# Kernel optimization log

Measured on AMD Instinct MI355X. Metric: run time of the kernel, lower is better.

The kernel has to match this reference:

```python
import jax, jax.numpy as jnp
import numpy as np

DIM = 1024
HEADS = 16
HEAD_DIM = DIM // HEADS
RANK = 4
AUDIO_DIM = 768


def _lora(x, A, B):
    # x: [..., in]; A: [rank, in]; B: [out, rank]
    return x + (x @ A.T @ B.T) * (1.0 / RANK)


def setup_inputs() -> dict:
    key = jax.random.key(0)
    ks = jax.random.split(key, 20)
    s = 0.02
    inp = {
        "x": jax.random.normal(ks[0], (1, 4096, DIM), jnp.float32),
        "audio_features": jax.random.normal(ks[1], (1, 1024, AUDIO_DIM), jnp.float32),
        "q_w": jax.random.normal(ks[2], (DIM, DIM), jnp.float32) * s,
        "q_b": jnp.zeros((DIM,), jnp.float32),
        "k_w": jax.random.normal(ks[3], (DIM, DIM), jnp.float32) * s,
        "k_b": jnp.zeros((DIM,), jnp.float32),
        "v_w": jax.random.normal(ks[4], (DIM, DIM), jnp.float32) * s,
        "v_b": jnp.zeros((DIM,), jnp.float32),
        "o_w": jax.random.normal(ks[5], (DIM, DIM), jnp.float32) * s,
        "o_b": jnp.zeros((DIM,), jnp.float32),
        "a_w": jax.random.normal(ks[6], (DIM, AUDIO_DIM), jnp.float32) * s,
        "a_b": jnp.zeros((DIM,), jnp.float32),
        "qA": jax.random.normal(ks[7], (RANK, DIM), jnp.float32) * 0.01,
        "qB": jax.random.normal(ks[8], (DIM, RANK), jnp.float32) * 0.01,
        "kA": jax.random.normal(ks[9], (RANK, DIM), jnp.float32) * 0.01,
        "kB": jax.random.normal(ks[10], (DIM, RANK), jnp.float32) * 0.01,
        "vA": jax.random.normal(ks[11], (RANK, DIM), jnp.float32) * 0.01,
        "vB": jax.random.normal(ks[12], (DIM, RANK), jnp.float32) * 0.01,
    }
    return inp


def reference(x, audio_features, q_w, q_b, k_w, k_b, v_w, v_b, o_w, o_b,
              a_w, a_b, qA, qB, kA, kB, vA, vB):
    B, N, C = x.shape
    # audio projection: Linear(768 -> dim), torch Linear is x @ W.T + b
    audio = audio_features @ a_w.T + a_b  # [B, M, C]
    M = audio.shape[1]

    q = _lora(x @ q_w.T + q_b, qA, qB)      # [B, N, C]
    k = _lora(audio @ k_w.T + k_b, kA, kB)  # [B, M, C]
    v = _lora(audio @ v_w.T + v_b, vA, vB)  # [B, M, C]

    q = q.reshape(B, N, HEADS, HEAD_DIM).transpose(0, 2, 1, 3)  # [B,H,N,d]
    k = k.reshape(B, M, HEADS, HEAD_DIM).transpose(0, 2, 1, 3)  # [B,H,M,d]
    v = v.reshape(B, M, HEADS, HEAD_DIM).transpose(0, 2, 1, 3)  # [B,H,M,d]

    scale = HEAD_DIM ** -0.5
    attn = jnp.einsum('bhnd,bhmd->bhnm', q, k) * scale  # [B,H,N,M]
    attn = jax.nn.softmax(attn, axis=-1)
    out = jnp.einsum('bhnm,bhmd->bhnd', attn, v)        # [B,H,N,d]
    out = out.transpose(0, 2, 1, 3).reshape(B, N, C)
    return out @ o_w.T + o_b
```

## Files before the change

### kernel.cpp

```cpp
#include <hip/hip_runtime.h>
#include <math.h>

#define DIM 1024
#define HEADS 16
#define HD 64

typedef __attribute__((ext_vector_type(8))) short short8;
typedef __attribute__((ext_vector_type(4))) float f32x4;
typedef unsigned short ushort_t;

#define MFMA(a, b, c) __builtin_amdgcn_mfma_f32_16x16x32_bf16(a, b, c, 0, 0, 0)
#define VMCNT(n) asm volatile("s_waitcnt vmcnt(" #n ")" ::: "memory")
#define BARRIER() __builtin_amdgcn_s_barrier()

#define QSCALE 0.1803368801111204f

__device__ __forceinline__ ushort_t f2bf(float f) {
    union { float f; unsigned u; } v; v.f = f;
    unsigned r = v.u + 0x7FFF + ((v.u >> 16) & 1);
    return (ushort_t)(r >> 16);
}
__device__ __forceinline__ float bf2f(ushort_t h) {
    union { unsigned u; float f; } v; v.u = ((unsigned)h) << 16;
    return v.f;
}
__device__ __forceinline__ void gl2lds16(const void* g, void* l) {
    __builtin_amdgcn_global_load_lds(
        (const __attribute__((address_space(1))) unsigned*)g,
        (__attribute__((address_space(3))) unsigned*)l, 16, 0, 0);
}

#define C_X  1048576
#define C_AF 196608
__global__ __launch_bounds__(256) void cvt_all(
    const float* __restrict__ x, const float* __restrict__ af,
    const float* __restrict__ aw, const float* __restrict__ ow,
    ushort_t* __restrict__ xb, ushort_t* __restrict__ afb,
    ushort_t* __restrict__ awb, ushort_t* __restrict__ owb)
{
    int c = blockIdx.x * 256 + threadIdx.x;
    const float* s; ushort_t* d; int off;
    if (c < C_X)                { s = x;  d = xb;  off = c; }
    else if (c < C_X + C_AF)    { s = af; d = afb; off = c - C_X; }
    else if (c < C_X + 2*C_AF)  { s = aw; d = awb; off = c - C_X - C_AF; }
    else                        { s = ow; d = owb; off = c - C_X - 2*C_AF; }
    float4 v = ((const float4*)s)[off];
    ushort4 o = { f2bf(v.x), f2bf(v.y), f2bf(v.z), f2bf(v.w) };
    ((ushort4*)d)[off] = o;
}

__global__ __launch_bounds__(256) void lora_wt_part(
    const float* __restrict__ qw, const float* __restrict__ kw,
    const float* __restrict__ vw, const float* __restrict__ qA,
    const float* __restrict__ kA, const float* __restrict__ vA,
    float* __restrict__ part)
{
    int proj = blockIdx.z >> 3, oc = blockIdx.z & 7;
    int r = blockIdx.y;
    int i = blockIdx.x * 256 + threadIdx.x;
    const float* W = proj == 0 ? qw : proj == 1 ? kw : vw;
    const float* A = proj == 0 ? qA : proj == 1 ? kA : vA;
    float s = 0.f;
    int o0 = oc * 128;
    for (int o = o0; o < o0 + 128; ++o)
        s = fmaf(A[r * 1024 + o], W[(size_t)o * 1024 + i], s);
    part[(size_t)(((proj * 8 + oc) * 4 + r) << 10) + i] = s;
}

__global__ __launch_bounds__(256) void lora_wt_reduce(
    const float* __restrict__ part, float* __restrict__ T1)
{
    int proj = blockIdx.z, r = blockIdx.y;
    int i = blockIdx.x * 256 + threadIdx.x;
    float s = 0.f;
    #pragma unroll
    for (int oc = 0; oc < 8; ++oc)
        s += part[(size_t)(((proj * 8 + oc) * 4 + r) << 10) + i];
    T1[(size_t)((proj * 4 + r) << 10) + i] = s;
}

__global__ __launch_bounds__(256) void lora_bt(
    const float* __restrict__ qb_, const float* __restrict__ kb_,
    const float* __restrict__ vb_, const float* __restrict__ qA,
    const float* __restrict__ kA, const float* __restrict__ vA,
    const float* __restrict__ qB, const float* __restrict__ kB,
    const float* __restrict__ vB, float* __restrict__ beff)
{
    int proj = blockIdx.x;
    const float* b = proj == 0 ? qb_ : proj == 1 ? kb_ : vb_;
    const float* A = proj == 0 ? qA : proj == 1 ? kA : vA;
    const float* B = proj == 0 ? qB : proj == 1 ? kB : vB;
    int tid = threadIdx.x, lane = tid & 63, w = tid >> 6;
    float t[4] = {0.f, 0.f, 0.f, 0.f};
    for (int o = tid; o < 1024; o += 256) {
        float bo = b[o];
        #pragma unroll
        for (int r = 0; r < 4; ++r) t[r] = fmaf(A[r * 1024 + o], bo, t[r]);
    }
    __shared__ float red[4][4];
    #pragma unroll
    for (int r = 0; r < 4; ++r) {
        float v = t[r];
        #pragma unroll
        for (int off = 32; off; off >>= 1) v += __shfl_xor(v, off);
        if (lane == 0) red[r][w] = v;
    }
    __syncthreads();
    float t0 = red[0][0] + red[0][1] + red[0][2] + red[0][3];
    float t1 = red[1][0] + red[1][1] + red[1][2] + red[1][3];
    float t2 = red[2][0] + red[2][1] + red[2][2] + red[2][3];
    float t3 = red[3][0] + red[3][1] + red[3][2] + red[3][3];
    for (int o = tid; o < 1024; o += 256) {
        float4 Bo = *(const float4*)(B + o * 4);
        beff[proj * 1024 + o] =
            b[o] + 0.25f * (Bo.x * t0 + Bo.y * t1 + Bo.z * t2 + Bo.w * t3);
    }
}

__global__ __launch_bounds__(256) void lora_wapply(
    const float* __restrict__ qw, const float* __restrict__ kw,
    const float* __restrict__ vw, const float* __restrict__ qB,
    const float* __restrict__ kB, const float* __restrict__ vB,
    const float* __restrict__ T1, ushort_t* __restrict__ Wq,
    ushort_t* __restrict__ Wk, ushort_t* __restrict__ Wv)
{
    int proj = blockIdx.y;
    const float* W = proj == 0 ? qw : proj == 1 ? kw : vw;
    const float* B = proj == 0 ? qB : proj == 1 ? kB : vB;
    ushort_t* Wo = proj == 0 ? Wq : proj == 1 ? Wk : Wv;
    int idx = (blockIdx.x * 256 + threadIdx.x) * 4;
    int o = idx >> 10, i = idx & 1023;
    float4 w = *(const float4*)(W + idx);
    float4 Bo = *(const float4*)(B + o * 4);
    const float* T = T1 + (proj << 12);
    float4 t0 = *(const float4*)(T + i);
    float4 t1 = *(const float4*)(T + 1024 + i);
    float4 t2 = *(const float4*)(T + 2048 + i);
    float4 t3 = *(const float4*)(T + 3072 + i);
    ushort4 out;
    out.x = f2bf(w.x + 0.25f * (Bo.x*t0.x + Bo.y*t1.x + Bo.z*t2.x + Bo.w*t3.x));
    out.y = f2bf(w.y + 0.25f * (Bo.x*t0.y + Bo.y*t1.y + Bo.z*t2.y + Bo.w*t3.y));
    out.z = f2bf(w.z + 0.25f * (Bo.x*t0.z + Bo.y*t1.z + Bo.z*t2.z + Bo.w*t3.z));
    out.w = f2bf(w.w + 0.25f * (Bo.x*t0.w + Bo.y*t1.w + Bo.z*t2.w + Bo.w*t3.w));
    *(ushort4*)(Wo + idx) = out;
}

template<int MFRAG, int OUTF32>
__global__ __launch_bounds__(256) void gemm2(
    const ushort_t* __restrict__ A, const ushort_t* __restrict__ W,
    const float* __restrict__ bias, void* __restrict__ C, int N, int K)
{
    constexpr int MT = MFRAG * 64;
    __shared__ ushort_t As[2][MT * 32];
    __shared__ ushort_t Ws[2][64 * 32];
    const int tid = threadIdx.x, lane = tid & 63, wv = tid >> 6;
    const int l15 = lane & 15, l4 = lane >> 4;
    const int bm = blockIdx.y, bn = blockIdx.x;

    const ushort_t* Ag[MFRAG];
    #pragma unroll
    for (int c = 0; c < MFRAG; ++c) {
        int f = c * 256 + tid, ra = f >> 2, ga = (f & 3) ^ ((ra >> 1) & 3);
        Ag[c] = A + (size_t)(bm * MT + ra) * K + ga * 8;
    }
    int fb = tid, rb = fb >> 2, gb = (fb & 3) ^ ((rb >> 1) & 3);
    const ushort_t* Wg = W + (size_t)(bn * 64 + rb) * K + gb * 8;

    int aoff[MFRAG], woff[4];
    #pragma unroll
    for (int m = 0; m < MFRAG; ++m) {
        int r = wv * (MFRAG * 16) + m * 16 + l15;
        aoff[m] = r * 64 + ((l4 ^ ((r >> 1) & 3)) << 4);
    }
    #pragma unroll
    for (int n = 0; n < 4; ++n) {
        int cc = n * 16 + l15;
        woff[n] = cc * 64 + ((l4 ^ ((cc >> 1) & 3)) << 4);
    }

    f32x4 acc[MFRAG][4] = {};
    const int nt = K / 32;

    #pragma unroll
    for (int c = 0; c < MFRAG; ++c)
        gl2lds16(Ag[c], (char*)As + (c * 4 + wv) * 1024);
    gl2lds16(Wg, (char*)Ws + wv * 1024);

    for (int t = 0; t < nt; ++t) {
        const int buf = t & 1;
        if (t + 1 < nt) {
            const int k1 = (t + 1) * 32;
            #pragma unroll
            for (int c = 0; c < MFRAG; ++c)
                gl2lds16(Ag[c] + k1,
                         (char*)As + (buf ^ 1) * (MT * 64) + (c * 4 + wv) * 1024);
            gl2lds16(Wg + k1, (char*)Ws + (buf ^ 1) * 4096 + wv * 1024);
            if (MFRAG == 2) { VMCNT(3); } else { VMCNT(2); }
        } else {
            VMCNT(0);
        }
        BARRIER();
        const char* AsB = (const char*)As + buf * (MT * 64);
        const char* WsB = (const char*)Ws + buf * 4096;
        short8 fa[MFRAG], fw[4];
        #pragma unroll
        for (int m = 0; m < MFRAG; ++m) fa[m] = *(const short8*)(AsB + aoff[m]);
        #pragma unroll
        for (int n = 0; n < 4; ++n) fw[n] = *(const short8*)(WsB + woff[n]);
        #pragma unroll
        for (int m = 0; m < MFRAG; ++m)
            #pragma unroll
            for (int n = 0; n < 4; ++n)
                acc[m][n] = MFMA(fa[m], fw[n], acc[m][n]);
        BARRIER();
    }

    #pragma unroll
    for (int n = 0; n < 4; ++n) {
        int gc = bn * 64 + n * 16 + l15;
        float bv = bias[gc];
        #pragma unroll
        for (int m = 0; m < MFRAG; ++m) {
            int gr = bm * MT + wv * (MFRAG * 16) + m * 16 + (l4 << 2);
            #pragma unroll
            for (int j = 0; j < 4; ++j) {
                float v = acc[m][n][j] + bv;
                if (OUTF32) ((float*)C)[(size_t)(gr + j) * N + gc] = v;
                else        ((ushort_t*)C)[(size_t)(gr + j) * N + gc] = f2bf(v);
            }
        }
    }
}

template<int OUTF32, int SCALEQ>
__global__ __launch_bounds__(256) void gemm3(
    const ushort_t* __restrict__ A, const ushort_t* __restrict__ W,
    const float* __restrict__ bias, void* __restrict__ C, int N, int K)
{
    __shared__ ushort_t As[2][128 * 32];
    __shared__ ushort_t Ws[2][128 * 32];
    const int tid = threadIdx.x, lane = tid & 63, wv = tid >> 6;
    const int l15 = lane & 15, l4 = lane >> 4;
    const int wm = wv >> 1, wn = wv & 1;
    const int bm = blockIdx.y, bn = blockIdx.x;

    const ushort_t *Ag[2], *Wg[2];
    #pragma unroll
    for (int c = 0; c < 2; ++c) {
        int f = c * 256 + tid, ra = f >> 2, ga = (f & 3) ^ ((ra >> 1) & 3);
        Ag[c] = A + (size_t)(bm * 128 + ra) * K + ga * 8;
        Wg[c] = W + (size_t)(bn * 128 + ra) * K + ga * 8;
    }

    int aoff[4], woff[4];
    #pragma unroll
    for (int m = 0; m < 4; ++m) {
        int r = wm * 64 + m * 16 + l15;
        aoff[m] = r * 64 + ((l4 ^ ((r >> 1) & 3)) << 4);
    }
    #pragma unroll
    for (int n = 0; n < 4; ++n) {
        int cc = wn * 64 + n * 16 + l15;
        woff[n] = cc * 64 + ((l4 ^ ((cc >> 1) & 3)) << 4);
    }

    f32x4 acc[4][4] = {};
    const int nt = K / 32;

    #pragma unroll
    for (int c = 0; c < 2; ++c) {
        gl2lds16(Ag[c], (char*)As + c * 4096 + wv * 1024);
        gl2lds16(Wg[c], (char*)Ws + c * 4096 + wv * 1024);
    }

    for (int t = 0; t < nt; ++t) {
        const int buf = t & 1;
        if (t + 1 < nt) {
            const int k1 = (t + 1) * 32;
            #pragma unroll
            for (int c = 0; c < 2; ++c) {
                gl2lds16(Ag[c] + k1, (char*)As + (buf ^ 1) * 8192 + c * 4096 + wv * 1024);
                gl2lds16(Wg[c] + k1, (char*)Ws + (buf ^ 1) * 8192 + c * 4096 + wv * 1024);
            }
            VMCNT(4);
        } else {
            VMCNT(0);
        }
        BARRIER();
        const char* AsB = (const char*)As + buf * 8192;
        const char* WsB = (const char*)Ws + buf * 8192;
        short8 fa[4], fw[4];
        #pragma unroll
        for (int m = 0; m < 4; ++m) fa[m] = *(const short8*)(AsB + aoff[m]);
        #pragma unroll
        for (int n = 0; n < 4; ++n) fw[n] = *(const short8*)(WsB + woff[n]);
        #pragma unroll
        for (int m = 0; m < 4; ++m)
            #pragma unroll
            for (int n = 0; n < 4; ++n)
                acc[m][n] = MFMA(fa[m], fw[n], acc[m][n]);
        BARRIER();
    }

    #pragma unroll
    for (int n = 0; n < 4; ++n) {
        int gc = bn * 128 + wn * 64 + n * 16 + l15;
        float bv = bias[gc];
        #pragma unroll
        for (int m = 0; m < 4; ++m) {
            int gr = bm * 128 + wm * 64 + m * 16 + (l4 << 2);
            #pragma unroll
            for (int j = 0; j < 4; ++j) {
                float v = acc[m][n][j] + bv;
                if (SCALEQ) v *= QSCALE;
                if (OUTF32) ((float*)C)[(size_t)(gr + j) * N + gc] = v;
                else        ((ushort_t*)C)[(size_t)(gr + j) * N + gc] = f2bf(v);
            }
        }
    }
}

__global__ __launch_bounds__(256) void gemm2_kv(
    const ushort_t* __restrict__ A, const ushort_t* __restrict__ Wk,
    const ushort_t* __restrict__ Wv, const float* __restrict__ bk,
    const float* __restrict__ bv, ushort_t* __restrict__ Ck,
    ushort_t* __restrict__ CvT)
{
    const int K = DIM;
    __shared__ ushort_t As[2][64 * 32];
    __shared__ ushort_t Ws[2][64 * 32];
    const int tid = threadIdx.x, lane = tid & 63, wv = tid >> 6;
    const int l15 = lane & 15, l4 = lane >> 4;
    const int bm = blockIdx.y;
    const bool isV = blockIdx.x >= 16;
    const int bn = blockIdx.x & 15;
    const ushort_t* W = isV ? Wv : Wk;

    int f = tid, ra = f >> 2, ga = (f & 3) ^ ((ra >> 1) & 3);
    const ushort_t* Ag = A + (size_t)(bm * 64 + ra) * K + ga * 8;
    const ushort_t* Wg = W + (size_t)(bn * 64 + ra) * K + ga * 8;

    int aoff, woff[4];
    {
        int r = wv * 16 + l15;
        aoff = r * 64 + ((l4 ^ ((r >> 1) & 3)) << 4);
    }
    #pragma unroll
    for (int n = 0; n < 4; ++n) {
        int cc = n * 16 + l15;
        woff[n] = cc * 64 + ((l4 ^ ((cc >> 1) & 3)) << 4);
    }

    f32x4 acc[4] = {};
    const int nt = K / 32;
    gl2lds16(Ag, (char*)As + wv * 1024);
    gl2lds16(Wg, (char*)Ws + wv * 1024);

    for (int t = 0; t < nt; ++t) {
        const int buf = t & 1;
        if (t + 1 < nt) {
            const int k1 = (t + 1) * 32;
            gl2lds16(Ag + k1, (char*)As + (buf ^ 1) * 4096 + wv * 1024);
            gl2lds16(Wg + k1, (char*)Ws + (buf ^ 1) * 4096 + wv * 1024);
            VMCNT(2);
        } else {
            VMCNT(0);
        }
        BARRIER();
        const char* AsB = (const char*)As + buf * 4096;
        const char* WsB = (const char*)Ws + buf * 4096;
        short8 fa = *(const short8*)(AsB + aoff);
        short8 fw[4];
        #pragma unroll
        for (int n = 0; n < 4; ++n) fw[n] = *(const short8*)(WsB + woff[n]);
        #pragma unroll
        for (int n = 0; n < 4; ++n) acc[n] = MFMA(fa, fw[n], acc[n]);
        BARRIER();
    }

    const int gr = bm * 64 + wv * 16 + (l4 << 2);
    #pragma unroll
    for (int n = 0; n < 4; ++n) {
        int gc = bn * 64 + n * 16 + l15;
        float bb = (isV ? bv : bk)[gc];
        if (!isV) {
            #pragma unroll
            for (int j = 0; j < 4; ++j)
                Ck[(size_t)(gr + j) * DIM + gc] = f2bf(acc[n][j] + bb);
        } else {
            ushort4 o = { f2bf(acc[n][0] + bb), f2bf(acc[n][1] + bb),
                          f2bf(acc[n][2] + bb), f2bf(acc[n][3] + bb) };
            *(ushort4*)(CvT + (size_t)gc * DIM + gr) = o;
        }
    }
}

__global__ __launch_bounds__(256) void attn3(
    const ushort_t* __restrict__ Qf, const ushort_t* __restrict__ Kf,
    const ushort_t* __restrict__ Vt, ushort_t* __restrict__ AO)
{
    __shared__ char lds[40960];
    char* QsPs = lds;
    char* KsB0 = lds + 8192;
    char* VsB0 = lds + 24576;

    const int tid = threadIdx.x, lane = tid & 63, wv = tid >> 6;
    const int l15 = lane & 15, l4 = lane >> 4;
    const int h = blockIdx.y, qb = blockIdx.x;

    #pragma unroll
    for (int i = 0; i < 2; ++i) {
        int f = i * 256 + tid, q = f >> 3, s = (f & 7) ^ (q & 7);
        gl2lds16(Qf + (size_t)(qb * 64 + q) * DIM + h * HD + s * 8,
                 QsPs + i * 4096 + wv * 1024);
    }
    const int f0 = tid, r0 = f0 >> 3, s0 = (f0 & 7) ^ (r0 & 7);
    const int f1 = 256 + tid, r1 = f1 >> 3, s1 = (f1 & 7) ^ (r1 & 7);
    const ushort_t* Kg0 = Kf + (size_t)r0 * DIM + h * HD + s0 * 8;
    const ushort_t* Kg1 = Kf + (size_t)r1 * DIM + h * HD + s1 * 8;
    const ushort_t* Vg0 = Vt + (size_t)(h * HD + r0) * DIM + s0 * 8;
    const ushort_t* Vg1 = Vt + (size_t)(h * HD + r1) * DIM + s1 * 8;

    int qoff[2], koff[4][2], poff[2];
    #pragma unroll
    for (int ks = 0; ks < 2; ++ks) {
        int r = wv * 16 + l15;
        qoff[ks] = r * 128 + (((ks * 4 + l4) ^ (r & 7)) << 4);
        poff[ks] = wv * 2048 + l15 * 128 + (((ks * 4 + l4) ^ (l15 & 7)) << 4);
    }
    #pragma unroll
    for (int n = 0; n < 4; ++n) {
        int kk = n * 16 + l15;
        #pragma unroll
        for (int ks = 0; ks < 2; ++ks)
            koff[n][ks] = kk * 128 + (((ks * 4 + l4) ^ (kk & 7)) << 4);
    }

    f32x4 acc_o[4] = {};
    float l_loc[4] = {0.f, 0.f, 0.f, 0.f};

    gl2lds16(Kg0, KsB0 + wv * 1024);
    gl2lds16(Kg1, KsB0 + 4096 + wv * 1024);
    gl2lds16(Vg0, VsB0 + wv * 1024);
    gl2lds16(Vg1, VsB0 + 4096 + wv * 1024);
    VMCNT(4);
    BARRIER();
    short8 fq[2];
    #pragma unroll
    for (int ks = 0; ks < 2; ++ks)
        fq[ks] = *(const short8*)(QsPs + qoff[ks]);

    for (int t = 0; t < 16; ++t) {
        const int buf = t & 1;
        if (t < 15) {
            gl2lds16(Kg0 + (size_t)(t + 1) * 64 * DIM,
                     KsB0 + (buf ^ 1) * 8192 + wv * 1024);
            gl2lds16(Kg1 + (size_t)(t + 1) * 64 * DIM,
                     KsB0 + (buf ^ 1) * 8192 + 4096 + wv * 1024);
            gl2lds16(Vg0 + (t + 1) * 64,
                     VsB0 + (buf ^ 1) * 8192 + wv * 1024);
            gl2lds16(Vg1 + (t + 1) * 64,
                     VsB0 + (buf ^ 1) * 8192 + 4096 + wv * 1024);
            VMCNT(4);
        } else {
            VMCNT(0);
        }
        BARRIER();

        const char* KsT = KsB0 + buf * 8192;
        const char* VsT = VsB0 + buf * 8192;

        f32x4 s_acc[4] = {};
        short8 fk[4][2];
        #pragma unroll
        for (int n = 0; n < 4; ++n)
            #pragma unroll
            for (int ks = 0; ks < 2; ++ks)
                fk[n][ks] = *(const short8*)(KsT + koff[n][ks]);
        #pragma unroll
        for (int n = 0; n < 4; ++n)
            #pragma unroll
            for (int ks = 0; ks < 2; ++ks)
                s_acc[n] = MFMA(fq[ks], fk[n][ks], s_acc[n]);

        #pragma unroll
        for (int j = 0; j < 4; ++j) {
            float p0 = exp2f(s_acc[0][j]);
            float p1 = exp2f(s_acc[1][j]);
            float p2 = exp2f(s_acc[2][j]);
            float p3 = exp2f(s_acc[3][j]);
            l_loc[j] += (p0 + p1) + (p2 + p3);
            int r16 = (l4 << 2) + j;
            int basb = wv * 2048 + r16 * 128;
            int sw = (r16 & 7) << 4;
            int kx = l15 * 2;
            *(ushort_t*)(QsPs + basb + ((0 * 32 + kx) ^ sw)) = f2bf(p0);
            *(ushort_t*)(QsPs + basb + ((1 * 32 + kx) ^ sw)) = f2bf(p1);
            *(ushort_t*)(QsPs + basb + ((2 * 32 + kx) ^ sw)) = f2bf(p2);
            *(ushort_t*)(QsPs + basb + ((3 * 32 + kx) ^ sw)) = f2bf(p3);
        }

        short8 pa[2], fv[4][2];
        #pragma unroll
        for (int ks = 0; ks < 2; ++ks)
            pa[ks] = *(const short8*)(QsPs + poff[ks]);
        #pragma unroll
        for (int n = 0; n < 4; ++n)
            #pragma unroll
            for (int ks = 0; ks < 2; ++ks)
                fv[n][ks] = *(const short8*)(VsT + koff[n][ks]);
        #pragma unroll
        for (int dn = 0; dn < 4; ++dn)
            #pragma unroll
            for (int ks = 0; ks < 2; ++ks)
                acc_o[dn] = MFMA(pa[ks], fv[dn][ks], acc_o[dn]);
        BARRIER();
    }

    #pragma unroll
    for (int j = 0; j < 4; ++j) {
        float l = l_loc[j];
        l += __shfl_xor(l, 1);
        l += __shfl_xor(l, 2);
        l += __shfl_xor(l, 4);
        l += __shfl_xor(l, 8);
        float inv = 1.0f / l;
        int q = qb * 64 + wv * 16 + (l4 << 2) + j;
        #pragma unroll
        for (int dn = 0; dn < 4; ++dn)
            AO[(size_t)q * DIM + h * HD + dn * 16 + l15] =
                f2bf(acc_o[dn][j] * inv);
    }
}

extern "C" void kernel_launch(void* const* d_in, const int* in_sizes, int n_in,
                              void* d_out, int out_size, void* d_ws, size_t ws_size,
                              hipStream_t stream)
{
    const float* x   = (const float*)d_in[0];
    const float* af  = (const float*)d_in[1];
    const float* q_w = (const float*)d_in[2];
    const float* q_b = (const float*)d_in[3];
    const float* k_w = (const float*)d_in[4];
    const float* k_b = (const float*)d_in[5];
    const float* v_w = (const float*)d_in[6];
    const float* v_b = (const float*)d_in[7];
    const float* o_w = (const float*)d_in[8];
    const float* o_b = (const float*)d_in[9];
    const float* a_w = (const float*)d_in[10];
    const float* a_b = (const float*)d_in[11];
    const float* qA  = (const float*)d_in[12];
    const float* qB  = (const float*)d_in[13];
    const float* kA  = (const float*)d_in[14];
    const float* kB  = (const float*)d_in[15];
    const float* vA  = (const float*)d_in[16];
    const float* vB  = (const float*)d_in[17];
    float* out = (float*)d_out;

    const int N = 4096, M = 1024;

    char* w = (char*)d_ws;
    auto alloc = [&](size_t bytes) {
        char* p = w; w += (bytes + 255) & ~(size_t)255; return p;
    };
    ushort_t* xb   = (ushort_t*)alloc((size_t)N * DIM * 2);
    ushort_t* afb  = (ushort_t*)alloc((size_t)M * 768 * 2);
    ushort_t* awb  = (ushort_t*)alloc((size_t)DIM * 768 * 2);
    ushort_t* owb  = (ushort_t*)alloc((size_t)DIM * DIM * 2);
    ushort_t* wqe  = (ushort_t*)alloc((size_t)DIM * DIM * 2);
    ushort_t* wke  = (ushort_t*)alloc((size_t)DIM * DIM * 2);
    ushort_t* wve  = (ushort_t*)alloc((size_t)DIM * DIM * 2);
    ushort_t* audio= (ushort_t*)alloc((size_t)M * DIM * 2);
    ushort_t* qbb  = (ushort_t*)alloc((size_t)N * DIM * 2);
    ushort_t* kbb  = (ushort_t*)alloc((size_t)M * DIM * 2);
    ushort_t* vt   = (ushort_t*)alloc((size_t)M * DIM * 2);
    ushort_t* ao   = (ushort_t*)alloc((size_t)N * DIM * 2);
    float* part = (float*)alloc((size_t)3 * 8 * 4 * 1024 * 4);
    float* T1   = (float*)alloc((size_t)3 * 4 * 1024 * 4);
    float* beff = (float*)alloc((size_t)3 * 1024 * 4);

    cvt_all<<<6656, 256, 0, stream>>>(x, af, a_w, o_w, xb, afb, awb, owb);
    lora_wt_part<<<dim3(4, 4, 24), 256, 0, stream>>>(q_w, k_w, v_w, qA, kA, vA, part);
    lora_wt_reduce<<<dim3(4, 4, 3), 256, 0, stream>>>(part, T1);
    lora_bt<<<3, 256, 0, stream>>>(q_b, k_b, v_b, qA, kA, vA, qB, kB, vB, beff);
    lora_wapply<<<dim3(1024, 3), 256, 0, stream>>>(q_w, k_w, v_w, qB, kB, vB,
                                                   T1, wqe, wke, wve);

    gemm2<1, 0><<<dim3(16, 16), 256, 0, stream>>>(afb, awb, a_b, audio, DIM, 768);
    gemm3<0, 1><<<dim3(8, 32), 256, 0, stream>>>(xb, wqe, beff, qbb, DIM, DIM);
    gemm2_kv<<<dim3(32, 16), 256, 0, stream>>>(audio, wke, wve,
                                               beff + 1024, beff + 2048, kbb, vt);
    attn3<<<dim3(N / 64, HEADS), 256, 0, stream>>>(qbb, kbb, vt, ao);
    gemm3<1, 0><<<dim3(8, 32), 256, 0, stream>>>(ao, owb, o_b, out, DIM, DIM);
}
```

Measured before the change: 239.4 us.

## Fuse prep kernels, merge audio and Q GEMMs, triple-buffer GEMM pipeline

The conversion, LoRA weight-fold, bias-fold and apply kernels are merged into one prep launch. The Q scale is folded into the effective Q weights and bias. The audio projection and Q projection GEMMs now run as a single launch with heterogeneous blocks, and the 128x128 GEMM moves to a three-stage LDS pipeline that prefetches fragments across the barrier. Attention packs P to bf16 with the hardware pk conversion. The goal is fewer launches and less load latency, at the cost of a serialised per-block LoRA reduction over 64 rows.

Result: faster. 227.3 us (-5.1%).

```diff
diff --git a/kernel.cpp b/kernel.cpp
--- a/kernel.cpp
+++ b/kernel.cpp
@@ -4,6 +4,7 @@
 #define DIM 1024
 #define HEADS 16
 #define HD 64
+#define QSCALE 0.1803368801111204f
 
 typedef __attribute__((ext_vector_type(8))) short short8;
 typedef __attribute__((ext_vector_type(4))) float f32x4;
@@ -12,18 +13,12 @@
 #define MFMA(a, b, c) __builtin_amdgcn_mfma_f32_16x16x32_bf16(a, b, c, 0, 0, 0)
 #define VMCNT(n) asm volatile("s_waitcnt vmcnt(" #n ")" ::: "memory")
 #define BARRIER() __builtin_amdgcn_s_barrier()
-
-#define QSCALE 0.1803368801111204f
 
 __device__ __forceinline__ ushort_t f2bf(float f) {
     union { float f; unsigned u; } v; v.f = f;
     unsigned r = v.u + 0x7FFF + ((v.u >> 16) & 1);
     return (ushort_t)(r >> 16);
 }
-__device__ __forceinline__ float bf2f(ushort_t h) {
-    union { unsigned u; float f; } v; v.u = ((unsigned)h) << 16;
-    return v.f;
-}
 __device__ __forceinline__ void gl2lds16(const void* g, void* l) {
     __builtin_amdgcn_global_load_lds(
         (const __attribute__((address_space(1))) unsigned*)g,
@@ -32,196 +27,187 @@
 
 #define C_X  1048576
 #define C_AF 196608
-__global__ __launch_bounds__(256) void cvt_all(
+__global__ __launch_bounds__(256) void prep_cvt(
     const float* __restrict__ x, const float* __restrict__ af,
     const float* __restrict__ aw, const float* __restrict__ ow,
     ushort_t* __restrict__ xb, ushort_t* __restrict__ afb,
-    ushort_t* __restrict__ awb, ushort_t* __restrict__ owb)
-{
-    int c = blockIdx.x * 256 + threadIdx.x;
-    const float* s; ushort_t* d; int off;
-    if (c < C_X)                { s = x;  d = xb;  off = c; }
-    else if (c < C_X + C_AF)    { s = af; d = afb; off = c - C_X; }
-    else if (c < C_X + 2*C_AF)  { s = aw; d = awb; off = c - C_X - C_AF; }
-    else                        { s = ow; d = owb; off = c - C_X - 2*C_AF; }
-    float4 v = ((const float4*)s)[off];
-    ushort4 o = { f2bf(v.x), f2bf(v.y), f2bf(v.z), f2bf(v.w) };
-    ((ushort4*)d)[off] = o;
-}
-
-__global__ __launch_bounds__(256) void lora_wt_part(
+    ushort_t* __restrict__ awb, ushort_t* __restrict__ owb,
     const float* __restrict__ qw, const float* __restrict__ kw,
-    const float* __restrict__ vw, const float* __restrict__ qA,
-    const float* __restrict__ kA, const float* __restrict__ vA,
-    float* __restrict__ part)
-{
-    int proj = blockIdx.z >> 3, oc = blockIdx.z & 7;
-    int r = blockIdx.y;
-    int i = blockIdx.x * 256 + threadIdx.x;
+    const float* __restrict__ vw,
+    const float* __restrict__ qA, const float* __restrict__ kA,
+    const float* __restrict__ vA,
+    const float* __restrict__ qB, const float* __restrict__ kB,
+    const float* __restrict__ vB,
+    const float* __restrict__ qb, const float* __restrict__ kb,
+    const float* __restrict__ vb,
+    ushort_t* __restrict__ wqe, ushort_t* __restrict__ wke,
+    ushort_t* __restrict__ wve, float* __restrict__ beff)
+{
+    const int b = blockIdx.x, tid = threadIdx.x;
+    if (b < 6656) {
+        int c = b * 256 + tid;
+        const float* s; ushort_t* d; int off;
+        if (c < C_X)               { s = x;  d = xb;  off = c; }
+        else if (c < C_X + C_AF)   { s = af; d = afb; off = c - C_X; }
+        else if (c < C_X + 2*C_AF) { s = aw; d = awb; off = c - C_X - C_AF; }
+        else                       { s = ow; d = owb; off = c - C_X - 2*C_AF; }
+        float4 v = ((const float4*)s)[off];
+        ushort4 o = { f2bf(v.x), f2bf(v.y), f2bf(v.z), f2bf(v.w) };
+        ((ushort4*)d)[off] = o;
+        return;
+    }
+    const int pb = b - 6656;
+    const int proj = pb >> 6, ib = pb & 63;
     const float* W = proj == 0 ? qw : proj == 1 ? kw : vw;
     const float* A = proj == 0 ? qA : proj == 1 ? kA : vA;
-    float s = 0.f;
-    int o0 = oc * 128;
-    for (int o = o0; o < o0 + 128; ++o)
-        s = fmaf(A[r * 1024 + o], W[(size_t)o * 1024 + i], s);
-    part[(size_t)(((proj * 8 + oc) * 4 + r) << 10) + i] = s;
-}
-
-__global__ __launch_bounds__(256) void lora_wt_reduce(
-    const float* __restrict__ part, float* __restrict__ T1)
-{
-    int proj = blockIdx.z, r = blockIdx.y;
-    int i = blockIdx.x * 256 + threadIdx.x;
-    float s = 0.f;
-    #pragma unroll
-    for (int oc = 0; oc < 8; ++oc)
-        s += part[(size_t)(((proj * 8 + oc) * 4 + r) << 10) + i];
-    T1[(size_t)((proj * 4 + r) << 10) + i] = s;
-}
-
-__global__ __launch_bounds__(256) void lora_bt(
-    const float* __restrict__ qb_, const float* __restrict__ kb_,
-    const float* __restrict__ vb_, const float* __restrict__ qA,
-    const float* __restrict__ kA, const float* __restrict__ vA,
-    const float* __restrict__ qB, const float* __restrict__ kB,
-    const float* __restrict__ vB, float* __restrict__ beff)
-{
-    int proj = blockIdx.x;
-    const float* b = proj == 0 ? qb_ : proj == 1 ? kb_ : vb_;
-    const float* A = proj == 0 ? qA : proj == 1 ? kA : vA;
     const float* B = proj == 0 ? qB : proj == 1 ? kB : vB;
-    int tid = threadIdx.x, lane = tid & 63, w = tid >> 6;
-    float t[4] = {0.f, 0.f, 0.f, 0.f};
-    for (int o = tid; o < 1024; o += 256) {
-        float bo = b[o];
-        #pragma unroll
-        for (int r = 0; r < 4; ++r) t[r] = fmaf(A[r * 1024 + o], bo, t[r]);
-    }
-    __shared__ float red[4][4];
-    #pragma unroll
-    for (int r = 0; r < 4; ++r) {
-        float v = t[r];
-        #pragma unroll
-        for (int off = 32; off; off >>= 1) v += __shfl_xor(v, off);
-        if (lane == 0) red[r][w] = v;
-    }
+    const float* bias = proj == 0 ? qb : proj == 1 ? kb : vb;
+    ushort_t* Weff = proj == 0 ? wqe : proj == 1 ? wke : wve;
+    const float scale = proj == 0 ? QSCALE : 1.0f;
+
+    const int ic = tid & 15;
+    const int oc = tid >> 4;
+    const int i = ib * 16 + ic;
+
+    float part[4] = {0.f, 0.f, 0.f, 0.f};
+    for (int o = oc * 64; o < oc * 64 + 64; ++o) {
+        float wv = W[(size_t)o * 1024 + i];
+        part[0] = fmaf(A[o], wv, part[0]);
+        part[1] = fmaf(A[1024 + o], wv, part[1]);
+        part[2] = fmaf(A[2048 + o], wv, part[2]);
+        part[3] = fmaf(A[3072 + o], wv, part[3]);
+    }
+    __shared__ float red[4][16][16];
+    #pragma unroll
+    for (int r = 0; r < 4; ++r) red[r][oc][ic] = part[r];
     __syncthreads();
-    float t0 = red[0][0] + red[0][1] + red[0][2] + red[0][3];
-    float t1 = red[1][0] + red[1][1] + red[1][2] + red[1][3];
-    float t2 = red[2][0] + red[2][1] + red[2][2] + red[2][3];
-    float t3 = red[3][0] + red[3][1] + red[3][2] + red[3][3];
-    for (int o = tid; o < 1024; o += 256) {
+    __shared__ float T1s[4][16];
+    if (tid < 64) {
+        int r = tid >> 4, icc = tid & 15;
+        float s = 0.f;
+        #pragma unroll
+        for (int u = 0; u < 16; ++u) s += red[r][u][icc];
+        T1s[r][icc] = s;
+    }
+    __syncthreads();
+    const float t0 = T1s[0][ic], t1 = T1s[1][ic];
+    const float t2 = T1s[2][ic], t3 = T1s[3][ic];
+    for (int o = oc * 64; o < oc * 64 + 64; ++o) {
         float4 Bo = *(const float4*)(B + o * 4);
-        beff[proj * 1024 + o] =
-            b[o] + 0.25f * (Bo.x * t0 + Bo.y * t1 + Bo.z * t2 + Bo.w * t3);
-    }
-}
-
-__global__ __launch_bounds__(256) void lora_wapply(
-    const float* __restrict__ qw, const float* __restrict__ kw,
-    const float* __restrict__ vw, const float* __restrict__ qB,
-    const float* __restrict__ kB, const float* __restrict__ vB,
-    const float* __restrict__ T1, ushort_t* __restrict__ Wq,
-    ushort_t* __restrict__ Wk, ushort_t* __restrict__ Wv)
-{
-    int proj = blockIdx.y;
-    const float* W = proj == 0 ? qw : proj == 1 ? kw : vw;
-    const float* B = proj == 0 ? qB : proj == 1 ? kB : vB;
-    ushort_t* Wo = proj == 0 ? Wq : proj == 1 ? Wk : Wv;
-    int idx = (blockIdx.x * 256 + threadIdx.x) * 4;
-    int o = idx >> 10, i = idx & 1023;
-    float4 w = *(const float4*)(W + idx);
-    float4 Bo = *(const float4*)(B + o * 4);
-    const float* T = T1 + (proj << 12);
-    float4 t0 = *(const float4*)(T + i);
-    float4 t1 = *(const float4*)(T + 1024 + i);
-    float4 t2 = *(const float4*)(T + 2048 + i);
-    float4 t3 = *(const float4*)(T + 3072 + i);
-    ushort4 out;
-    out.x = f2bf(w.x + 0.25f * (Bo.x*t0.x + Bo.y*t1.x + Bo.z*t2.x + Bo.w*t3.x));
-    out.y = f2bf(w.y + 0.25f * (Bo.x*t0.y + Bo.y*t1.y + Bo.z*t2.y + Bo.w*t3.y));
-    out.z = f2bf(w.z + 0.25f * (Bo.x*t0.z + Bo.y*t1.z + Bo.z*t2.z + Bo.w*t3.z));
-    out.w = f2bf(w.w + 0.25f * (Bo.x*t0.w + Bo.y*t1.w + Bo.z*t2.w + Bo.w*t3.w));
-    *(ushort4*)(Wo + idx) = out;
-}
-
-template<int MFRAG, int OUTF32>
-__global__ __launch_bounds__(256) void gemm2(
-    const ushort_t* __restrict__ A, const ushort_t* __restrict__ W,
-    const float* __restrict__ bias, void* __restrict__ C, int N, int K)
-{
-    constexpr int MT = MFRAG * 64;
-    __shared__ ushort_t As[2][MT * 32];
-    __shared__ ushort_t Ws[2][64 * 32];
+        float wv = W[(size_t)o * 1024 + i];
+        float v = wv + 0.25f * (Bo.x*t0 + Bo.y*t1 + Bo.z*t2 + Bo.w*t3);
+        Weff[(size_t)o * 1024 + i] = f2bf(v * scale);
+    }
+    if (ib == 0) {
+        float bt[4] = {0.f, 0.f, 0.f, 0.f};
+        for (int o = tid; o < 1024; o += 256) {
+            float bo = bias[o];
+            bt[0] = fmaf(A[o], bo, bt[0]);
+            bt[1] = fmaf(A[1024 + o], bo, bt[1]);
+            bt[2] = fmaf(A[2048 + o], bo, bt[2]);
+            bt[3] = fmaf(A[3072 + o], bo, bt[3]);
+        }
+        #pragma unroll
+        for (int r = 0; r < 4; ++r)
+            #pragma unroll
+            for (int off = 32; off; off >>= 1) bt[r] += __shfl_xor(bt[r], off);
+        __shared__ float btr[4][4];
+        if ((tid & 63) == 0) {
+            #pragma unroll
+            for (int r = 0; r < 4; ++r) btr[r][tid >> 6] = bt[r];
+        }
+        __syncthreads();
+        float b0 = btr[0][0] + btr[0][1] + btr[0][2] + btr[0][3];
+        float b1 = btr[1][0] + btr[1][1] + btr[1][2] + btr[1][3];
+        float b2 = btr[2][0] + btr[2][1] + btr[2][2] + btr[2][3];
+        float b3 = btr[3][0] + btr[3][1] + btr[3][2] + btr[3][3];
+        for (int o = tid; o < 1024; o += 256) {
+            float4 Bo = *(const float4*)(B + o * 4);
+            beff[proj * 1024 + o] =
+                (bias[o] + 0.25f * (Bo.x*b0 + Bo.y*b1 + Bo.z*b2 + Bo.w*b3)) * scale;
+        }
+    }
+}
+
+template<int OUTF32>
+__device__ __forceinline__ void gemm3p_body(
+    char* lds, const ushort_t* __restrict__ A, const ushort_t* __restrict__ W,
+    const float* __restrict__ bias, void* __restrict__ C,
+    int N, int K, int bm, int bn)
+{
     const int tid = threadIdx.x, lane = tid & 63, wv = tid >> 6;
     const int l15 = lane & 15, l4 = lane >> 4;
-    const int bm = blockIdx.y, bn = blockIdx.x;
-
-    const ushort_t* Ag[MFRAG];
-    #pragma unroll
-    for (int c = 0; c < MFRAG; ++c) {
+    const int wm = wv >> 1, wn = wv & 1;
+
+    const ushort_t *Ag[2], *Wg[2];
+    #pragma unroll
+    for (int c = 0; c < 2; ++c) {
         int f = c * 256 + tid, ra = f >> 2, ga = (f & 3) ^ ((ra >> 1) & 3);
-        Ag[c] = A + (size_t)(bm * MT + ra) * K + ga * 8;
-    }
-    int fb = tid, rb = fb >> 2, gb = (fb & 3) ^ ((rb >> 1) & 3);
-    const ushort_t* Wg = W + (size_t)(bn * 64 + rb) * K + gb * 8;
-
-    int aoff[MFRAG], woff[4];
-    #pragma unroll
-    for (int m = 0; m < MFRAG; ++m) {
-        int r = wv * (MFRAG * 16) + m * 16 + l15;
+        Ag[c] = A + (size_t)(bm * 128 + ra) * K + ga * 8;
+        Wg[c] = W + (size_t)(bn * 128 + ra) * K + ga * 8;
+    }
+    int aoff[4], woff[4];
+    #pragma unroll
+    for (int m = 0; m < 4; ++m) {
+        int r = wm * 64 + m * 16 + l15;
         aoff[m] = r * 64 + ((l4 ^ ((r >> 1) & 3)) << 4);
     }
     #pragma unroll
     for (int n = 0; n < 4; ++n) {
-        int cc = n * 16 + l15;
+        int cc = wn * 64 + n * 16 + l15;
         woff[n] = cc * 64 + ((l4 ^ ((cc >> 1) & 3)) << 4);
     }
 
-    f32x4 acc[MFRAG][4] = {};
+    auto stage = [&](char* base, int k0) {
+        #pragma unroll
+        for (int c = 0; c < 2; ++c) {
+            gl2lds16(Ag[c] + k0, base + c * 4096 + wv * 1024);
+            gl2lds16(Wg[c] + k0, base + 8192 + c * 4096 + wv * 1024);
+        }
+    };
+
+    short8 fa[4], fw[4];
+    auto readfr = [&](const char* base) {
+        #pragma unroll
+        for (int m = 0; m < 4; ++m) fa[m] = *(const short8*)(base + aoff[m]);
+        #pragma unroll
+        for (int n = 0; n < 4; ++n) fw[n] = *(const short8*)(base + 8192 + woff[n]);
+    };
+
+    f32x4 acc[4][4] = {};
     const int nt = K / 32;
 
-    #pragma unroll
-    for (int c = 0; c < MFRAG; ++c)
-        gl2lds16(Ag[c], (char*)As + (c * 4 + wv) * 1024);
-    gl2lds16(Wg, (char*)Ws + wv * 1024);
-
+    stage(lds, 0);
+    stage(lds + 16384, 32);
+    VMCNT(4);
+    BARRIER();
+    readfr(lds);
+
+    int bcur = 0;
     for (int t = 0; t < nt; ++t) {
-        const int buf = t & 1;
-        if (t + 1 < nt) {
-            const int k1 = (t + 1) * 32;
-            #pragma unroll
-            for (int c = 0; c < MFRAG; ++c)
-                gl2lds16(Ag[c] + k1,
-                         (char*)As + (buf ^ 1) * (MT * 64) + (c * 4 + wv) * 1024);
-            gl2lds16(Wg + k1, (char*)Ws + (buf ^ 1) * 4096 + wv * 1024);
-            if (MFRAG == 2) { VMCNT(3); } else { VMCNT(2); }
-        } else {
-            VMCNT(0);
-        }
-        BARRIER();
-        const char* AsB = (const char*)As + buf * (MT * 64);
-        const char* WsB = (const char*)Ws + buf * 4096;
-        short8 fa[MFRAG], fw[4];
-        #pragma unroll
-        for (int m = 0; m < MFRAG; ++m) fa[m] = *(const short8*)(AsB + aoff[m]);
-        #pragma unroll
-        for (int n = 0; n < 4; ++n) fw[n] = *(const short8*)(WsB + woff[n]);
-        #pragma unroll
-        for (int m = 0; m < MFRAG; ++m)
+        int bnext = bcur + 1; if (bnext == 3) bnext = 0;
+        int bpre  = bnext + 1; if (bpre == 3) bpre = 0;
+        if (t + 2 < nt) stage(lds + bpre * 16384, (t + 2) * 32);
+        #pragma unroll
+        for (int m = 0; m < 4; ++m)
             #pragma unroll
             for (int n = 0; n < 4; ++n)
                 acc[m][n] = MFMA(fa[m], fw[n], acc[m][n]);
-        BARRIER();
-    }
-
-    #pragma unroll
-    for (int n = 0; n < 4; ++n) {
-        int gc = bn * 64 + n * 16 + l15;
+        if (t + 1 < nt) {
+            if (t + 2 < nt) { VMCNT(4); } else { VMCNT(0); }
+            BARRIER();
+            readfr(lds + bnext * 16384);
+        }
+        bcur = bnext;
+    }
+
+    #pragma unroll
+    for (int n = 0; n < 4; ++n) {
+        int gc = bn * 128 + wn * 64 + n * 16 + l15;
         float bv = bias[gc];
         #pragma unroll
-        for (int m = 0; m < MFRAG; ++m) {
-            int gr = bm * MT + wv * (MFRAG * 16) + m * 16 + (l4 << 2);
+        for (int m = 0; m < 4; ++m) {
+            int gr = bm * 128 + wm * 64 + m * 16 + (l4 << 2);
             #pragma unroll
             for (int j = 0; j < 4; ++j) {
                 float v = acc[m][n][j] + bv;
@@ -232,91 +218,88 @@
     }
 }
 
-template<int OUTF32, int SCALEQ>
-__global__ __launch_bounds__(256) void gemm3(
+template<int OUTF32>
+__global__ __launch_bounds__(256) void gemm3p(
     const ushort_t* __restrict__ A, const ushort_t* __restrict__ W,
     const float* __restrict__ bias, void* __restrict__ C, int N, int K)
 {
-    __shared__ ushort_t As[2][128 * 32];
-    __shared__ ushort_t Ws[2][128 * 32];
+    __shared__ char lds[49152];
+    gemm3p_body<OUTF32>(lds, A, W, bias, C, N, K, blockIdx.y, blockIdx.x);
+}
+
+__device__ __forceinline__ void audio_body(
+    char* lds, const ushort_t* __restrict__ A, const ushort_t* __restrict__ W,
+    const float* __restrict__ bias, ushort_t* __restrict__ C, int bm, int bn)
+{
+    const int K = 768, N = DIM;
+    char* As = lds;
+    char* Ws = lds + 8192;
     const int tid = threadIdx.x, lane = tid & 63, wv = tid >> 6;
     const int l15 = lane & 15, l4 = lane >> 4;
-    const int wm = wv >> 1, wn = wv & 1;
-    const int bm = blockIdx.y, bn = blockIdx.x;
-
-    const ushort_t *Ag[2], *Wg[2];
-    #pragma unroll
-    for (int c = 0; c < 2; ++c) {
-        int f = c * 256 + tid, ra = f >> 2, ga = (f & 3) ^ ((ra >> 1) & 3);
-        Ag[c] = A + (size_t)(bm * 128 + ra) * K + ga * 8;
-        Wg[c] = W + (size_t)(bn * 128 + ra) * K + ga * 8;
-    }
-
-    int aoff[4], woff[4];
-    #pragma unroll
-    for (int m = 0; m < 4; ++m) {
-        int r = wm * 64 + m * 16 + l15;
-        aoff[m] = r * 64 + ((l4 ^ ((r >> 1) & 3)) << 4);
-    }
-    #pragma unroll
-    for (int n = 0; n < 4; ++n) {
-        int cc = wn * 64 + n * 16 + l15;
+
+    int f = tid, ra = f >> 2, ga = (f & 3) ^ ((ra >> 1) & 3);
+    const ushort_t* Ag = A + (size_t)(bm * 64 + ra) * K + ga * 8;
+    const ushort_t* Wg = W + (size_t)(bn * 64 + ra) * K + ga * 8;
+
+    int aoff, woff[4];
+    { int r = wv * 16 + l15; aoff = r * 64 + ((l4 ^ ((r >> 1) & 3)) << 4); }
+    #pragma unroll
+    for (int n = 0; n < 4; ++n) {
+        int cc = n * 16 + l15;
         woff[n] = cc * 64 + ((l4 ^ ((cc >> 1) & 3)) << 4);
     }
 
-    f32x4 acc[4][4] = {};
+    f32x4 acc[4] = {};
     const int nt = K / 32;
-
-    #pragma unroll
-    for (int c = 0; c < 2; ++c) {
-        gl2lds16(Ag[c], (char*)As + c * 4096 + wv * 1024);
-        gl2lds16(Wg[c], (char*)Ws + c * 4096 + wv * 1024);
-    }
+    gl2lds16(Ag, As + wv * 1024);
+    gl2lds16(Wg, Ws + wv * 1024);
 
     for (int t = 0; t < nt; ++t) {
         const int buf = t & 1;
         if (t + 1 < nt) {
             const int k1 = (t + 1) * 32;
-            #pragma unroll
-            for (int c = 0; c < 2; ++c) {
-                gl2lds16(Ag[c] + k1, (char*)As + (buf ^ 1) * 8192 + c * 4096 + wv * 1024);
-                gl2lds16(Wg[c] + k1, (char*)Ws + (buf ^ 1) * 8192 + c * 4096 + wv * 1024);
-            }
-            VMCNT(4);
+            gl2lds16(Ag + k1, As + (buf ^ 1) * 4096 + wv * 1024);
+            gl2lds16(Wg + k1, Ws + (buf ^ 1) * 4096 + wv * 1024);
+            VMCNT(2);
         } else {
             VMCNT(0);
         }
         BARRIER();
-        const char* AsB = (const char*)As + buf * 8192;
-        const char* WsB = (const char*)Ws + buf * 8192;
-        short8 fa[4], fw[4];
-        #pragma unroll
-        for (int m = 0; m < 4; ++m) fa[m] = *(const short8*)(AsB + aoff[m]);
+        const char* AsB = As + buf * 4096;
+        const char* WsB = Ws + buf * 4096;
+        short8 fa = *(const short8*)(AsB + aoff);
+        short8 fw[4];
         #pragma unroll
         for (int n = 0; n < 4; ++n) fw[n] = *(const short8*)(WsB + woff[n]);
         #pragma unroll
-        for (int m = 0; m < 4; ++m)
-            #pragma unroll
-            for (int n = 0; n < 4; ++n)
-                acc[m][n] = MFMA(fa[m], fw[n], acc[m][n]);
+        for (int n = 0; n < 4; ++n) acc[n] = MFMA(fa, fw[n], acc[n]);
         BARRIER();
     }
 
-    #pragma unroll
-    for (int n = 0; n < 4; ++n) {
-        int gc = bn * 128 + wn * 64 + n * 16 + l15;
-        float bv = bias[gc];
-        #pragma unroll
-        for (int m = 0; m < 4; ++m) {
-            int gr = bm * 128 + wm * 64 + m * 16 + (l4 << 2);
-            #pragma unroll
-            for (int j = 0; j < 4; ++j) {
-                float v = acc[m][n][j] + bv;
-                if (SCALEQ) v *= QSCALE;
-                if (OUTF32) ((float*)C)[(size_t)(gr + j) * N + gc] = v;
-                else        ((ushort_t*)C)[(size_t)(gr + j) * N + gc] = f2bf(v);
-            }
-        }
+    const int gr = bm * 64 + wv * 16 + (l4 << 2);
+    #pragma unroll
+    for (int n = 0; n < 4; ++n) {
+        int gc = bn * 64 + n * 16 + l15;
+        float bb = bias[gc];
+        #pragma unroll
+        for (int j = 0; j < 4; ++j)
+            C[(size_t)(gr + j) * N + gc] = f2bf(acc[n][j] + bb);
+    }
+}
+
+__global__ __launch_bounds__(256) void fused_aq(
+    const ushort_t* __restrict__ afb, const ushort_t* __restrict__ awb,
+    const float* __restrict__ a_b, ushort_t* __restrict__ audio,
+    const ushort_t* __restrict__ xb, const ushort_t* __restrict__ wqe,
+    const float* __restrict__ beff, ushort_t* __restrict__ qbb)
+{
+    __shared__ char lds[49152];
+    const int b = blockIdx.x;
+    if (b < 256) {
+        audio_body(lds, afb, awb, a_b, audio, b >> 4, b & 15);
+    } else {
+        const int i = b - 256;
+        gemm3p_body<0>(lds, xb, wqe, beff, qbb, DIM, DIM, i >> 3, i & 7);
     }
 }
 
@@ -341,10 +324,7 @@
     const ushort_t* Wg = W + (size_t)(bn * 64 + ra) * K + ga * 8;
 
     int aoff, woff[4];
-    {
-        int r = wv * 16 + l15;
-        aoff = r * 64 + ((l4 ^ ((r >> 1) & 3)) << 4);
-    }
+    { int r = wv * 16 + l15; aoff = r * 64 + ((l4 ^ ((r >> 1) & 3)) << 4); }
     #pragma unroll
     for (int n = 0; n < 4; ++n) {
         int cc = n * 16 + l15;
@@ -490,14 +470,17 @@
             float p2 = exp2f(s_acc[2][j]);
             float p3 = exp2f(s_acc[3][j]);
             l_loc[j] += (p0 + p1) + (p2 + p3);
+            unsigned pk01, pk23;
+            asm("v_cvt_pk_bf16_f32 %0, %1, %2" : "=v"(pk01) : "v"(p0), "v"(p1));
+            asm("v_cvt_pk_bf16_f32 %0, %1, %2" : "=v"(pk23) : "v"(p2), "v"(p3));
             int r16 = (l4 << 2) + j;
             int basb = wv * 2048 + r16 * 128;
             int sw = (r16 & 7) << 4;
             int kx = l15 * 2;
-            *(ushort_t*)(QsPs + basb + ((0 * 32 + kx) ^ sw)) = f2bf(p0);
-            *(ushort_t*)(QsPs + basb + ((1 * 32 + kx) ^ sw)) = f2bf(p1);
-            *(ushort_t*)(QsPs + basb + ((2 * 32 + kx) ^ sw)) = f2bf(p2);
-            *(ushort_t*)(QsPs + basb + ((3 * 32 + kx) ^ sw)) = f2bf(p3);
+            *(ushort_t*)(QsPs + basb + ((kx) ^ sw))      = (ushort_t)pk01;
+            *(ushort_t*)(QsPs + basb + ((32 + kx) ^ sw)) = (ushort_t)(pk01 >> 16);
+            *(ushort_t*)(QsPs + basb + ((64 + kx) ^ sw)) = (ushort_t)pk23;
+            *(ushort_t*)(QsPs + basb + ((96 + kx) ^ sw)) = (ushort_t)(pk23 >> 16);
         }
 
         short8 pa[2], fv[4][2];
@@ -557,39 +540,33 @@
     const float* vB  = (const float*)d_in[17];
     float* out = (float*)d_out;
 
-    const int N = 4096, M = 1024;
+    const int N = 4096;
 
     char* w = (char*)d_ws;
     auto alloc = [&](size_t bytes) {
         char* p = w; w += (bytes + 255) & ~(size_t)255; return p;
     };
     ushort_t* xb   = (ushort_t*)alloc((size_t)N * DIM * 2);
-    ushort_t* afb  = (ushort_t*)alloc((size_t)M * 768 * 2);
+    ushort_t* afb  = (ushort_t*)alloc((size_t)1024 * 768 * 2);
     ushort_t* awb  = (ushort_t*)alloc((size_t)DIM * 768 * 2);
     ushort_t* owb  = (ushort_t*)alloc((size_t)DIM * DIM * 2);
     ushort_t* wqe  = (ushort_t*)alloc((size_t)DIM * DIM * 2);
     ushort_t* wke  = (ushort_t*)alloc((size_t)DIM * DIM * 2);
     ushort_t* wve  = (ushort_t*)alloc((size_t)DIM * DIM * 2);
-    ushort_t* audio= (ushort_t*)alloc((size_t)M * DIM * 2);
+    ushort_t* audio= (ushort_t*)alloc((size_t)1024 * DIM * 2);
     ushort_t* qbb  = (ushort_t*)alloc((size_t)N * DIM * 2);
-    ushort_t* kbb  = (ushort_t*)alloc((size_t)M * DIM * 2);
-    ushort_t* vt   = (ushort_t*)alloc((size_t)M * DIM * 2);
+    ushort_t* kbb  = (ushort_t*)alloc((size_t)1024 * DIM * 2);
+    ushort_t* vt   = (ushort_t*)alloc((size_t)1024 * DIM * 2);
     ushort_t* ao   = (ushort_t*)alloc((size_t)N * DIM * 2);
-    float* part = (float*)alloc((size_t)3 * 8 * 4 * 1024 * 4);
-    float* T1   = (float*)alloc((size_t)3 * 4 * 1024 * 4);
     float* beff = (float*)alloc((size_t)3 * 1024 * 4);
 
-    cvt_all<<<6656, 256, 0, stream>>>(x, af, a_w, o_w, xb, afb, awb, owb);
-    lora_wt_part<<<dim3(4, 4, 24), 256, 0, stream>>>(q_w, k_w, v_w, qA, kA, vA, part);
-    lora_wt_reduce<<<dim3(4, 4, 3), 256, 0, stream>>>(part, T1);
-    lora_bt<<<3, 256, 0, stream>>>(q_b, k_b, v_b, qA, kA, vA, qB, kB, vB, beff);
-    lora_wapply<<<dim3(1024, 3), 256, 0, stream>>>(q_w, k_w, v_w, qB, kB, vB,
-                                                   T1, wqe, wke, wve);
-
-    gemm2<1, 0><<<dim3(16, 16), 256, 0, stream>>>(afb, awb, a_b, audio, DIM, 768);
-    gemm3<0, 1><<<dim3(8, 32), 256, 0, stream>>>(xb, wqe, beff, qbb, DIM, DIM);
+    prep_cvt<<<6848, 256, 0, stream>>>(
+        x, af, a_w, o_w, xb, afb, awb, owb,
+        q_w, k_w, v_w, qA, kA, vA, qB, kB, vB, q_b, k_b, v_b,
+        wqe, wke, wve, beff);
+    fused_aq<<<512, 256, 0, stream>>>(afb, awb, a_b, audio, xb, wqe, beff, qbb);
     gemm2_kv<<<dim3(32, 16), 256, 0, stream>>>(audio, wke, wve,
                                                beff + 1024, beff + 2048, kbb, vt);
     attn3<<<dim3(N / 64, HEADS), 256, 0, stream>>>(qbb, kbb, vt, ao);
-    gemm3<1, 0><<<dim3(8, 32), 256, 0, stream>>>(ao, owb, o_b, out, DIM, DIM);
-}
+    gemm3p<1><<<dim3(8, 32), 256, 0, stream>>>(ao, owb, o_b, out, DIM, DIM);
+}
```
